# Performance work log

Measured on AMD Instinct MI355X. Metric: run time of the kernel, lower is better.

Reference implementation:

```python
import jax, jax.numpy as jnp
import numpy as np

N, L, C, NHEAD = 4, 2048, 1024, 8
D = C // NHEAD
EPS_ATTN = 1e-6
EPS_LN = 1e-5


def _w(key, shape, scale=0.02):
    return jax.random.normal(key, shape, dtype=jnp.float32) * scale


def setup_inputs() -> dict:
    key = jax.random.key(0)
    ks = jax.random.split(key, 32)
    inp = {
        'depth_feat': jax.random.normal(ks[0], (N, L, C), dtype=jnp.float32),
        'context_feat': jax.random.normal(ks[1], (N, L, C), dtype=jnp.float32),
        'depth_pos': jax.random.normal(ks[2], (N, L, C), dtype=jnp.float32),
        # encoder params (weights stored [in, out]; y = x @ W)
        'e_wq': _w(ks[3], (C, C)), 'e_wk': _w(ks[4], (C, C)), 'e_wv': _w(ks[5], (C, C)),
        'e_wm': _w(ks[6], (C, C)),
        'e_w1': _w(ks[7], (C, 2 * C)), 'e_w2': _w(ks[8], (2 * C, C)),
        'e_g1': jnp.ones((C,), jnp.float32), 'e_b1': jnp.zeros((C,), jnp.float32),
        'e_g2': jnp.ones((C,), jnp.float32), 'e_b2': jnp.zeros((C,), jnp.float32),
        # decoder params
        'd_wq0': _w(ks[9], (C, C)), 'd_wk0': _w(ks[10], (C, C)), 'd_wv0': _w(ks[11], (C, C)),
        'd_wm0': _w(ks[12], (C, C)),
        'd_wq1': _w(ks[13], (C, C)), 'd_wk1': _w(ks[14], (C, C)), 'd_wv1': _w(ks[15], (C, C)),
        'd_wm1': _w(ks[16], (C, C)),
        'd_w1': _w(ks[17], (C, 2 * C)), 'd_w2': _w(ks[18], (2 * C, C)),
        'd_g0': jnp.ones((C,), jnp.float32), 'd_b0': jnp.zeros((C,), jnp.float32),
        'd_g1': jnp.ones((C,), jnp.float32), 'd_b1': jnp.zeros((C,), jnp.float32),
        'd_g2': jnp.ones((C,), jnp.float32), 'd_b2': jnp.zeros((C,), jnp.float32),
    }
    return inp


def layernorm(x, g, b):
    m = jnp.mean(x, axis=-1, keepdims=True)
    v = jnp.mean(jnp.square(x - m), axis=-1, keepdims=True)
    return (x - m) * jax.lax.rsqrt(v + EPS_LN) * g + b


def linear_attention(q, k, v):
    # q,k,v: [N, L, H, D]; elu+1 feature map, O(L) kernelized attention
    Q = jax.nn.elu(q) + 1.0
    K = jax.nn.elu(k) + 1.0
    vlen = v.shape[1]
    v = v / vlen
    KV = jnp.einsum('nshd,nshv->nhdv', K, v)                    # [N,H,D,D]
    Z = 1.0 / (jnp.einsum('nlhd,nhd->nlh', Q, K.sum(axis=1)) + EPS_ATTN)
    out = jnp.einsum('nlhd,nhdv,nlh->nlhv', Q, KV, Z) * vlen    # [N,L,H,D]
    return out


def heads(x):
    n, l, c = x.shape
    return x.reshape(n, l, NHEAD, D)


def encoder_layer(x, wq, wk, wv, wm, w1, w2, g1, b1, g2, b2):
    n, l, c = x.shape
    msg = linear_attention(heads(x @ wq), heads(x @ wk), heads(x @ wv))
    msg = msg.reshape(n, l, c) @ wm
    x = x + layernorm(msg, g1, b1)
    x = x + layernorm(jax.nn.relu(x @ w1) @ w2, g2, b2)
    return x


def decoder_layer(x, src, wq0, wk0, wv0, wm0, wq1, wk1, wv1, wm1, w1, w2, g0, b0, g1, b1, g2, b2):
    n, l, c = x.shape
    msg = linear_attention(heads(x @ wq0), heads(x @ wk0), heads(x @ wv0))
    msg = msg.reshape(n, l, c) @ wm0
    x = x + layernorm(msg, g0, b0)
    msg = linear_attention(heads(x @ wq1), heads(src @ wk1), heads(src @ wv1))
    msg = msg.reshape(n, l, c) @ wm1
    x = x + layernorm(msg, g1, b1)
    x = x + layernorm(jax.nn.relu(x @ w1) @ w2, g2, b2)
    return x


def reference(depth_feat, context_feat, depth_pos,
              e_wq, e_wk, e_wv, e_wm, e_w1, e_w2, e_g1, e_b1, e_g2, e_b2,
              d_wq0, d_wk0, d_wv0, d_wm0, d_wq1, d_wk1, d_wv1, d_wm1,
              d_w1, d_w2, d_g0, d_b0, d_g1, d_b1, d_g2, d_b2):
    ctx = context_feat + depth_pos
    ctx = encoder_layer(ctx, e_wq, e_wk, e_wv, e_wm, e_w1, e_w2, e_g1, e_b1, e_g2, e_b2)
    out = decoder_layer(depth_feat, ctx,
                        d_wq0, d_wk0, d_wv0, d_wm0,
                        d_wq1, d_wk1, d_wv1, d_wm1,
                        d_w1, d_w2, d_g0, d_b0, d_g1, d_b1, d_g2, d_b2)
    return out
```

## Files before the change

### kernel.cpp

```cpp
#include <hip/hip_runtime.h>
#include <cstdint>

#define N_B 4
#define L_S 2048
#define C_F 1024
#define H_N 8
#define D_H 128
#define M_T (N_B * L_S)

typedef __bf16 bf16;
typedef __bf16 bf16x4 __attribute__((ext_vector_type(4)));
typedef __bf16 bf16x8 __attribute__((ext_vector_type(8)));
typedef float f32x4 __attribute__((ext_vector_type(4)));

typedef __attribute__((address_space(1))) void gvoid_t;
typedef __attribute__((address_space(3))) void lvoid_t;

__device__ __forceinline__ void lds_cp16(void* lds, const void* g) {
    __builtin_amdgcn_global_load_lds((gvoid_t*)g, (lvoid_t*)lds, 16, 0, 0);
}

__device__ __forceinline__ float elup1(float x) {
    return x > 0.0f ? x + 1.0f : __expf(x);
}

__device__ __forceinline__ void load4f(const void* base, size_t e0, int isbf, float* o) {
    if (isbf) {
        bf16x4 v = *(const bf16x4*)((const bf16*)base + e0);
        o[0] = (float)v[0]; o[1] = (float)v[1]; o[2] = (float)v[2]; o[3] = (float)v[3];
    } else {
        float4 v = *(const float4*)((const float*)base + e0);
        o[0] = v.x; o[1] = v.y; o[2] = v.z; o[3] = v.w;
    }
}

__device__ __forceinline__ int xcd_swz(int wgid, int nwg) {
    return (wgid & 7) * (nwg >> 3) + (wgid >> 3);
}

__global__ void detect_dtype(const unsigned int* g1, int* flag) {
    if (threadIdx.x == 0 && blockIdx.x == 0)
        *flag = (g1[0] == 0x3F803F80u) ? 1 : 0;
}

__global__ __launch_bounds__(256) void transpose_any(
        const void* __restrict__ src, bf16* __restrict__ dst,
        int R, int Cc, const int* __restrict__ flagp) {
    const int isbf = *flagp;
    __shared__ bf16 tile[32][33];
    const int bx = blockIdx.x * 32;
    const int by = blockIdx.y * 32;
    const int tx = threadIdx.x & 31;
    const int ty = threadIdx.x >> 5;
#pragma unroll
    for (int i = 0; i < 32; i += 8) {
        size_t ix = (size_t)(by + ty + i) * Cc + bx + tx;
        float v = isbf ? (float)((const bf16*)src)[ix] : ((const float*)src)[ix];
        tile[ty + i][tx] = (bf16)v;
    }
    __syncthreads();
#pragma unroll
    for (int i = 0; i < 32; i += 8)
        dst[(size_t)(bx + ty + i) * R + by + tx] = tile[tx][ty + i];
}

struct TAll {
    const void* src[16];
    unsigned int dstoff[16];
    int R[16];
    int C[16];
    int tile0[17];
};

__global__ __launch_bounds__(256) void transpose_all(
        TAll p, bf16* __restrict__ twall, const int* __restrict__ flagp) {
    const int isbf = *flagp;
    int gid = blockIdx.x;
    int w = 0;
    while (gid >= p.tile0[w + 1]) ++w;
    const int local = gid - p.tile0[w];
    const int R = p.R[w], Cc = p.C[w];
    const int tilesx = Cc >> 5;
    const int bx = (local % tilesx) * 32;
    const int by = (local / tilesx) * 32;
    const void* src = p.src[w];
    bf16* dst = twall + p.dstoff[w];
    __shared__ bf16 tile[32][33];
    const int tx = threadIdx.x & 31;
    const int ty = threadIdx.x >> 5;
#pragma unroll
    for (int i = 0; i < 32; i += 8) {
        size_t ix = (size_t)(by + ty + i) * Cc + bx + tx;
        float v = isbf ? (float)((const bf16*)src)[ix] : ((const float*)src)[ix];
        tile[ty + i][tx] = (bf16)v;
    }
    __syncthreads();
#pragma unroll
    for (int i = 0; i < 32; i += 8)
        dst[(size_t)(bx + ty + i) * R + by + tx] = tile[tx][ty + i];
}

template <int ACT>
__global__ __launch_bounds__(256, 2) void gemm_bt(
        const bf16* __restrict__ A, const bf16* __restrict__ Bt,
        bf16* __restrict__ C, int M, int N, int K) {
    __shared__ bf16 sA[2][128 * 64];
    __shared__ bf16 sB[2][128 * 64];
    const int t = threadIdx.x;
    const int lane = t & 63;
    const int w = t >> 6;
    const int wm = (w >> 1) * 64, wn = (w & 1) * 64;
    const int lr = lane & 15, lq = lane >> 4;
    const int gx = gridDim.x;
    const int nwg = gx * gridDim.y;
    const int wgid = xcd_swz(blockIdx.y * gx + blockIdx.x, nwg);
    const int m0 = (wgid / gx) * 128, n0 = (wgid % gx) * 128;

    const bf16* Ab = A + (size_t)m0 * K;
    const bf16* Bb = Bt + (size_t)n0 * K;

    f32x4 acc[4][4] = {};

#define GSTAGE(buf, kt)                                                       \
    {                                                                         \
        _Pragma("unroll")                                                     \
        for (int i_ = 0; i_ < 4; ++i_) {                                      \
            int ci_ = t + i_ * 256;                                           \
            int r_ = ci_ >> 3, c8_ = (ci_ & 7) * 8;                           \
            lds_cp16(&sA[buf][ci_ * 8], Ab + (size_t)r_ * K + (kt) + c8_);    \
        }                                                                     \
        _Pragma("unroll")                                                     \
        for (int i_ = 0; i_ < 4; ++i_) {                                      \
            int ci_ = t + i_ * 256;                                           \
            int r_ = ci_ >> 3, c8_ = (ci_ & 7) * 8;                           \
            lds_cp16(&sB[buf][ci_ * 8], Bb + (size_t)r_ * K + (kt) + c8_);    \
        }                                                                     \
    }

    GSTAGE(0, 0)
    __syncthreads();

    int b = 0;
    for (int kt = 0; kt < K; kt += 64, b ^= 1) {
        if (kt + 64 < K) GSTAGE(b ^ 1, kt + 64)
#pragma unroll
        for (int kk = 0; kk < 64; kk += 32) {
            bf16x8 af[4], bfr[4];
#pragma unroll
            for (int mi = 0; mi < 4; ++mi)
                af[mi] = *(const bf16x8*)&sA[b][(wm + mi * 16 + lr) * 64 + kk + lq * 8];
#pragma unroll
            for (int ni = 0; ni < 4; ++ni)
                bfr[ni] = *(const bf16x8*)&sB[b][(wn + ni * 16 + lr) * 64 + kk + lq * 8];
#pragma unroll
            for (int mi = 0; mi < 4; ++mi)
#pragma unroll
                for (int ni = 0; ni < 4; ++ni)
                    acc[mi][ni] = __builtin_amdgcn_mfma_f32_16x16x32_bf16(
                        af[mi], bfr[ni], acc[mi][ni], 0, 0, 0);
        }
        __syncthreads();
    }
#undef GSTAGE
#pragma unroll
    for (int mi = 0; mi < 4; ++mi)
#pragma unroll
        for (int ni = 0; ni < 4; ++ni)
#pragma unroll
            for (int r = 0; r < 4; ++r) {
                int row = m0 + wm + mi * 16 + lq * 4 + r;
                int col = n0 + wn + ni * 16 + lr;
                float v = acc[mi][ni][r];
                if (ACT == 1) v = fmaxf(v, 0.0f);
                if (ACT == 2) v = v > 0.0f ? v + 1.0f : __expf(v);
                C[(size_t)row * N + col] = (bf16)v;
            }
}

#define STAGE_T(sarr, Gbase, ldstride, Tt)                                    \
    {                                                                         \
        const int sl_ = (Tt) & 3;                                             \
        _Pragma("unroll")                                                     \
        for (int i_ = 0; i_ < 2; ++i_) {                                      \
            int ci_ = t + i_ * 512;                                           \
            int r_ = ci_ >> 2, c8_ = (ci_ & 3) * 8;                           \
            lds_cp16(&sarr[sl_ * 8192 + ci_ * 8],                             \
                     (Gbase) + (size_t)r_ * (ldstride) + ((Tt) << 5) +        \
                         (c8_ ^ ((r_ & 3) << 3)));                            \
        }                                                                     \
    }

template <int ACT>
__global__ __launch_bounds__(512, 2) void gemm256(
        const bf16* __restrict__ A, const bf16* __restrict__ Bt,
        bf16* __restrict__ C, int M, int N, int K, int actsplit) {
    __shared__ bf16 sA[4 * 256 * 32];
    __shared__ bf16 sB[4 * 256 * 32];
    const int t = threadIdx.x;
    const int lane = t & 63;
    const int w = t >> 6;
    const int wr = w >> 2, wc = w & 3;
    const int lr = lane & 15, lq = lane >> 4;
    const int gx = gridDim.x;
    const int nwg = gx * gridDim.y;
    const int wgid = xcd_swz(blockIdx.y * gx + blockIdx.x, nwg);
    const int m0 = (wgid / gx) * 256, n0 = (wgid % gx) * 256;
    const int nt = K >> 5;

    const bf16* Ab = A + (size_t)m0 * K;
    const bf16* Bb = Bt + (size_t)n0 * K;

    f32x4 acc[8][4] = {};

    STAGE_T(sA, Ab, K, 0); STAGE_T(sB, Bb, K, 0);
    STAGE_T(sA, Ab, K, 1); STAGE_T(sB, Bb, K, 1);
    asm volatile("s_waitcnt vmcnt(4)" ::: "memory");
    __builtin_amdgcn_s_barrier();

    for (int T = 0; T < nt; ++T) {
        const bf16* sAs = &sA[(T & 3) * 8192];
        const bf16* sBs = &sB[(T & 3) * 8192];
        bf16x8 af[4], bfr[4], ag[4];
#pragma unroll
        for (int mi = 0; mi < 4; ++mi) {
            int row = wr * 128 + mi * 16 + lr;
            af[mi] = *(const bf16x8*)&sAs[row * 32 + ((lq * 8) ^ ((row & 3) << 3))];
        }
#pragma unroll
        for (int ni = 0; ni < 4; ++ni) {
            int row = wc * 64 + ni * 16 + lr;
            bfr[ni] = *(const bf16x8*)&sBs[row * 32 + ((lq * 8) ^ ((row & 3) << 3))];
        }
        if (T + 2 < nt) STAGE_T(sA, Ab, K, T + 2);
        __builtin_amdgcn_s_barrier();
        __builtin_amdgcn_s_setprio(1);
#pragma unroll
        for (int mi = 0; mi < 4; ++mi)
#pragma unroll
            for (int ni = 0; ni < 4; ++ni)
                acc[mi][ni] = __builtin_amdgcn_mfma_f32_16x16x32_bf16(
                    af[mi], bfr[ni], acc[mi][ni], 0, 0, 0);
        __builtin_amdgcn_s_setprio(0);
        __builtin_amdgcn_s_barrier();
#pragma unroll
        for (int mi = 0; mi < 4; ++mi) {
            int row = wr * 128 + (mi + 4) * 16 + lr;
            ag[mi] = *(const bf16x8*)&sAs[row * 32 + ((lq * 8) ^ ((row & 3) << 3))];
        }
        if (T + 2 < nt) STAGE_T(sB, Bb, K, T + 2);
        __builtin_amdgcn_s_barrier();
        __builtin_amdgcn_s_setprio(1);
#pragma unroll
        for (int mi = 0; mi < 4; ++mi)
#pragma unroll
            for (int ni = 0; ni < 4; ++ni)
                acc[mi + 4][ni] = __builtin_amdgcn_mfma_f32_16x16x32_bf16(
                    ag[mi], bfr[ni], acc[mi + 4][ni], 0, 0, 0);
        __builtin_amdgcn_s_setprio(0);
        if (T + 1 < nt) {
            if (T + 2 < nt) asm volatile("s_waitcnt vmcnt(4)" ::: "memory");
            else            asm volatile("s_waitcnt vmcnt(0)" ::: "memory");
        }
        __builtin_amdgcn_s_barrier();
    }
#pragma unroll
    for (int mi = 0; mi < 8; ++mi)
#pragma unroll
        for (int ni = 0; ni < 4; ++ni)
#pragma unroll
            for (int r = 0; r < 4; ++r) {
                int row = m0 + wr * 128 + mi * 16 + lq * 4 + r;
                int col = n0 + wc * 64 + ni * 16 + lr;
                float v = acc[mi][ni][r];
                if (ACT == 1) v = fmaxf(v, 0.0f);
                if (ACT == 3 && row < actsplit) v = v > 0.0f ? v + 1.0f : __expf(v);
                C[(size_t)row * N + col] = (bf16)v;
            }
}

__global__ __launch_bounds__(256, 2) void attn_kv_mfma(
        const bf16* __restrict__ ktg, const bf16* __restrict__ vtg,
        bf16* __restrict__ KVp, float* __restrict__ KSp) {
    const int nh = blockIdx.x;
    const int chunk = blockIdx.y;
    const int n = nh >> 3, h = nh & 7;
    const int t = threadIdx.x;
    const int lane = t & 63;
    const int w = t >> 6;
    const int wm = (w >> 1) * 64, wn = (w & 1) * 64;
    const int lr = lane & 15, lq = lane >> 4;
    __shared__ bf16 sA[2][128 * 64];
    __shared__ bf16 sB[2][128 * 64];
    const size_t base = (size_t)(h * D_H) * M_T + (size_t)n * L_S + chunk * 128;
    const bf16* Ag0 = vtg + base;
    const bf16* Bg0 = ktg + base;

    f32x4 acc[4][4] = {};
    float ks = 0.0f;
    const int dh = t >> 1, half = (t & 1) * 32;

#define KVSTG(buf, kt)                                                        \
    {                                                                         \
        _Pragma("unroll")                                                     \
        for (int i_ = 0; i_ < 4; ++i_) {                                      \
            int ci_ = t + i_ * 256;                                           \
            int r_ = ci_ >> 3, c8_ = (ci_ & 7) * 8;                           \
            lds_cp16(&sA[buf][ci_ * 8], Ag0 + (size_t)r_ * M_T + (kt) + c8_); \
        }                                                                     \
        _Pragma("unroll")                                                     \
        for (int i_ = 0; i_ < 4; ++i_) {                                      \
            int ci_ = t + i_ * 256;                                           \
            int r_ = ci_ >> 3, c8_ = (ci_ & 7) * 8;                           \
            lds_cp16(&sB[buf][ci_ * 8], Bg0 + (size_t)r_ * M_T + (kt) + c8_); \
        }                                                                     \
    }

    KVSTG(0, 0)
    __syncthreads();

    int b = 0;
    for (int kt = 0; kt < 128; kt += 64, b ^= 1) {
        if (kt + 64 < 128) KVSTG(b ^ 1, kt + 64)
#pragma unroll
        for (int j = 0; j < 4; ++j) {
            bf16x8 v = *(const bf16x8*)&sB[b][dh * 64 + half + j * 8];
#pragma unroll
            for (int m = 0; m < 8; ++m) ks += (float)v[m];
        }
#pragma unroll
        for (int kk = 0; kk < 64; kk += 32) {
            bf16x8 af[4], bfr[4];
#pragma unroll
            for (int mi = 0; mi < 4; ++mi)
                af[mi] = *(const bf16x8*)&sA[b][(wm + mi * 16 + lr) * 64 + kk + lq * 8];
#pragma unroll
            for (int ni = 0; ni < 4; ++ni)
                bfr[ni] = *(const bf16x8*)&sB[b][(wn + ni * 16 + lr) * 64 + kk + lq * 8];
#pragma unroll
            for (int mi = 0; mi < 4; ++mi)
#pragma unroll
                for (int ni = 0; ni < 4; ++ni)
                    acc[mi][ni] = __builtin_amdgcn_mfma_f32_16x16x32_bf16(
                        af[mi], bfr[ni], acc[mi][ni], 0, 0, 0);
        }
        __syncthreads();
    }
#undef KVSTG
    float ko = __shfl_xor(ks, 1);
    if (!(t & 1)) KSp[(nh * 16 + chunk) * D_H + dh] = ks + ko;

    bf16* out = KVp + ((size_t)(nh * 16 + chunk)) * (D_H * D_H);
#pragma unroll
    for (int mi = 0; mi < 4; ++mi)
#pragma unroll
        for (int ni = 0; ni < 4; ++ni)
#pragma unroll
            for (int r = 0; r < 4; ++r) {
                int row = wm + mi * 16 + lq * 4 + r;
                int col = wn + ni * 16 + lr;
                out[(size_t)row * D_H + col] = (bf16)acc[mi][ni][r];
            }
}

__global__ __launch_bounds__(256) void attn_reduce_t(
        const bf16* __restrict__ KVp, const float* __restrict__ KSp,
        bf16* __restrict__ KVt, float* __restrict__ Ksum) {
    const int nh = blockIdx.x;
    const int es = blockIdx.y;
    const int t = threadIdx.x;
    const size_t base = (size_t)nh * 16 * (D_H * D_H) + es * 4096 + t * 16;
    float fa[16] = {};
    for (int c = 0; c < 16; ++c) {
        const bf16* p = KVp + base + (size_t)c * (D_H * D_H);
        bf16x8 a = *(const bf16x8*)p;
        bf16x8 b = *(const bf16x8*)(p + 8);
#pragma unroll
        for (int m = 0; m < 8; ++m) { fa[m] += (float)a[m]; fa[8 + m] += (float)b[m]; }
    }
    bf16* o = KVt + (size_t)nh * (D_H * D_H) + es * 4096 + t * 16;
    bf16x8 oa, ob;
#pragma unroll
    for (int m = 0; m < 8; ++m) { oa[m] = (bf16)fa[m]; ob[m] = (bf16)fa[8 + m]; }
    *(bf16x8*)o = oa;
    *(bf16x8*)(o + 8) = ob;
    if (es == 0 && t < 128) {
        float s = 0.0f;
#pragma unroll
        for (int c = 0; c < 16; ++c) s += KSp[(nh * 16 + c) * D_H + t];
        Ksum[nh * D_H + t] = s;
    }
}

__global__ __launch_bounds__(256, 2) void attn_out_mfma(
        const bf16* __restrict__ qb, const bf16* __restrict__ KVt,
        const float* __restrict__ Ksum, bf16* __restrict__ ab) {
    const int nh = blockIdx.x, tile = blockIdx.y;
    const int n = nh >> 3, h = nh & 7;
    const int t = threadIdx.x;
    const int lane = t & 63;
    const int w = t >> 6;
    const int wm = (w >> 1) * 64, wn = (w & 1) * 64;
    const int lr = lane & 15, lq = lane >> 4;
    __shared__ bf16 sA[2][128 * 64];
    __shared__ bf16 sB[2][128 * 64];
    __shared__ float sKs[128];
    __shared__ float sZp[128][2];
    __shared__ float sZ[128];
    if (t < 128) sKs[t] = Ksum[nh * D_H + t];

    f32x4 acc[4][4] = {};
    float zacc = 0.0f;
    const int zrow = t >> 1, zoff = (t & 1) * 32;
    const size_t qbase = ((size_t)(n * L_S + tile * 128)) * C_F + h * D_H;
    const bf16* Bg0 = KVt + (size_t)nh * (D_H * D_H);

#define OSTG(buf, kt)                                                         \
    {                                                                         \
        _Pragma("unroll")                                                     \
        for (int i_ = 0; i_ < 4; ++i_) {                                      \
            int ci_ = t + i_ * 256;                                           \
            int r_ = ci_ >> 3, c8_ = (ci_ & 7) * 8;                           \
            lds_cp16(&sA[buf][ci_ * 8],                                       \
                     qb + qbase + (size_t)r_ * C_F + (kt) + c8_);             \
            lds_cp16(&sB[buf][ci_ * 8], Bg0 + (size_t)r_ * D_H + (kt) + c8_); \
        }                                                                     \
    }

    OSTG(0, 0)
    __syncthreads();

    int b = 0;
    for (int kt = 0; kt < 128; kt += 64, b ^= 1) {
        if (kt + 64 < 128) OSTG(b ^ 1, kt + 64)
#pragma unroll 8
        for (int j = 0; j < 32; ++j)
            zacc += (float)sA[b][zrow * 64 + zoff + j] * sKs[kt + zoff + j];
#pragma unroll
        for (int kk = 0; kk < 64; kk += 32) {
            bf16x8 af[4], bfr[4];
#pragma unroll
            for (int mi = 0; mi < 4; ++mi)
                af[mi] = *(const bf16x8*)&sA[b][(wm + mi * 16 + lr) * 64 + kk + lq * 8];
#pragma unroll
            for (int ni = 0; ni < 4; ++ni)
                bfr[ni] = *(const bf16x8*)&sB[b][(wn + ni * 16 + lr) * 64 + kk + lq * 8];
#pragma unroll
            for (int mi = 0; mi < 4; ++mi)
#pragma unroll
                for (int ni = 0; ni < 4; ++ni)
                    acc[mi][ni] = __builtin_amdgcn_mfma_f32_16x16x32_bf16(
                        af[mi], bfr[ni], acc[mi][ni], 0, 0, 0);
        }
        __syncthreads();
    }
#undef OSTG
    sZp[zrow][t & 1] = zacc;
    __syncthreads();
    if (t < 128) sZ[t] = 1.0f / (sZp[t][0] + sZp[t][1] + 1e-6f);
    __syncthreads();
#pragma unroll
    for (int mi = 0; mi < 4; ++mi)
#pragma unroll
        for (int ni = 0; ni < 4; ++ni)
#pragma unroll
            for (int r = 0; r < 4; ++r) {
                int row = wm + mi * 16 + lq * 4 + r;
                int col = wn + ni * 16 + lr;
                ab[qbase + (size_t)row * C_F + col] = (bf16)(acc[mi][ni][r] * sZ[row]);
            }
}

template <int F32OUT>
__global__ __launch_bounds__(256) void ln_res(
        const bf16* __restrict__ msg, const void* __restrict__ g,
        const void* __restrict__ bb, const int* __restrict__ flagp,
        const bf16* __restrict__ xin, void* __restrict__ xout) {
    const int isbf = *flagp;
    const int row = blockIdx.x * 4 + (threadIdx.x >> 6);
    const int lane = threadIdx.x & 63;
    const size_t base = (size_t)row * C_F;
    float m[16];
#pragma unroll
    for (int k = 0; k < 4; ++k) {
        bf16x4 v = *(const bf16x4*)(msg + base + k * 256 + lane * 4);
        m[k * 4 + 0] = (float)v[0]; m[k * 4 + 1] = (float)v[1];
        m[k * 4 + 2] = (float)v[2]; m[k * 4 + 3] = (float)v[3];
    }
    float s1 = 0.0f, s2 = 0.0f;
#pragma unroll
    for (int q = 0; q < 16; ++q) { s1 += m[q]; s2 += m[q] * m[q]; }
#pragma unroll
    for (int off = 32; off > 0; off >>= 1) {
        s1 += __shfl_down(s1, off);
        s2 += __shfl_down(s2, off);
    }
    s1 = __shfl(s1, 0);
    s2 = __shfl(s2, 0);
    const float mean = s1 / C_F;
    const float rs = rsqrtf(s2 / C_F - mean * mean + 1e-5f);
#pragma unroll
    for (int k = 0; k < 4; ++k) {
        const size_t cix = k * 256 + lane * 4;
        float ga[4], ba[4];
        load4f(g, cix, isbf, ga);
        load4f(bb, cix, isbf, ba);
        bf16x4 x4 = *(const bf16x4*)(xin + base + cix);
        if (F32OUT) {
            float4 of;
            of.x = (float)x4[0] + (m[k * 4 + 0] - mean) * rs * ga[0] + ba[0];
            of.y = (float)x4[1] + (m[k * 4 + 1] - mean) * rs * ga[1] + ba[1];
            of.z = (float)x4[2] + (m[k * 4 + 2] - mean) * rs * ga[2] + ba[2];
            of.w = (float)x4[3] + (m[k * 4 + 3] - mean) * rs * ga[3] + ba[3];
            *(float4*)((float*)xout + base + cix) = of;
        } else {
            bf16x4 ob;
            ob[0] = (bf16)((float)x4[0] + (m[k * 4 + 0] - mean) * rs * ga[0] + ba[0]);
            ob[1] = (bf16)((float)x4[1] + (m[k * 4 + 1] - mean) * rs * ga[1] + ba[1]);
            ob[2] = (bf16)((float)x4[2] + (m[k * 4 + 2] - mean) * rs * ga[2] + ba[2]);
            ob[3] = (bf16)((float)x4[3] + (m[k * 4 + 3] - mean) * rs * ga[3] + ba[3]);
            *(bf16x4*)((bf16*)xout + base + cix) = ob;
        }
    }
}

__global__ __launch_bounds__(256) void init_ctx_kernel(
        const void* __restrict__ a, const void* __restrict__ b,
        const int* __restrict__ flagp, bf16* __restrict__ xb) {
    const int isbf = *flagp;
    const size_t i = ((size_t)blockIdx.x * 256 + threadIdx.x) * 4;
    float av[4], bv[4];
    load4f(a, i, isbf, av);
    load4f(b, i, isbf, bv);
    bf16x4 o;
#pragma unroll
    for (int q = 0; q < 4; ++q) o[q] = (bf16)(av[q] + bv[q]);
    *(bf16x4*)(xb + i) = o;
}

__global__ __launch_bounds__(256) void conv_copy_kernel(
        const void* __restrict__ a, const int* __restrict__ flagp,
        bf16* __restrict__ xb) {
    const int isbf = *flagp;
    const size_t i = ((size_t)blockIdx.x * 256 + threadIdx.x) * 4;
    float av[4];
    load4f(a, i, isbf, av);
    bf16x4 o;
#pragma unroll
    for (int q = 0; q < 4; ++q) o[q] = (bf16)av[q];
    *(bf16x4*)(xb + i) = o;
}

extern "C" void kernel_launch(void* const* d_in, const int* in_sizes, int n_in,
                              void* d_out, int out_size, void* d_ws, size_t ws_size,
                              hipStream_t stream) {
    const size_t MB = 1u << 20;
    uint8_t* W = (uint8_t*)d_ws;
    bf16* xb    = (bf16*)(W + 0);
    bf16* ctxb  = (bf16*)(W + 16 * MB);
    bf16* qb    = (bf16*)(W + 32 * MB);
    bf16* kb    = (bf16*)(W + 48 * MB);
    bf16* vb    = (bf16*)(W + 64 * MB);
    bf16* hb    = kb;
    bf16* S     = (bf16*)(W + 80 * MB);
    bf16* TW    = (bf16*)(W + 96 * MB);
    bf16* KVp   = S;
    float* KSp  = (float*)(W + 100 * MB);
    bf16* KVt   = (bf16*)(W + 101 * MB);
    float* Ksum = (float*)(W + 102 * MB);
    int*   flag = (int*)(W + 102 * MB + 64 * 1024);
    bf16* TWall = (bf16*)(W + 104 * MB);
    const bool batched = (ws_size >= 145 * MB);

    detect_dtype<<<1, 64, 0, stream>>>((const unsigned int*)d_in[9], flag);

    const int widx[16] = {3,4,5,6,7,8,13,14,15,16,17,18,19,20,21,22};
    const int wR[16]   = {1024,1024,1024,1024,1024,2048,1024,1024,1024,1024,
                          1024,1024,1024,1024,1024,2048};
    const int wC[16]   = {1024,1024,1024,1024,2048,1024,1024,1024,1024,1024,
                          1024,1024,1024,1024,2048,1024};
    unsigned int off[16];
    {
        unsigned int acc = 0;
        for (int i = 0; i < 16; ++i) { off[i] = acc; acc += (unsigned int)wR[i] * wC[i]; }
    }
    if (batched) {
        TAll p;
        int tacc = 0;
        for (int i = 0; i < 16; ++i) {
            p.src[i] = d_in[widx[i]];
            p.dstoff[i] = off[i];
            p.R[i] = wR[i];
            p.C[i] = wC[i];
            p.tile0[i] = tacc;
            tacc += (wR[i] / 32) * (wC[i] / 32);
        }
        p.tile0[16] = tacc;
        transpose_all<<<tacc, 256, 0, stream>>>(p, TWall, flag);
    }
    auto SLOT = [&](int idx) {
        for (int i = 0; i < 16; ++i) if (widx[i] == idx) return i;
        return 0;
    };
    auto BT = [&](int idx) -> const bf16* {
        int s = SLOT(idx);
        if (batched) return TWall + off[s];
        dim3 g(wC[s] / 32, wR[s] / 32);
        transpose_any<<<g, 256, 0, stream>>>(d_in[idx], TW, wR[s], wC[s], flag);
        return TW;
    };
    auto TG = [&](int idx, const bf16* A, bf16* Cc, int Nn, int Kk, int act) {
        const bf16* Bt = BT(idx);
        dim3 g(Nn / 128, M_T / 128);
        if (act == 1)      gemm_bt<1><<<g, 256, 0, stream>>>(A, Bt, Cc, M_T, Nn, Kk);
        else if (act == 2) gemm_bt<2><<<g, 256, 0, stream>>>(A, Bt, Cc, M_T, Nn, Kk);
        else               gemm_bt<0><<<g, 256, 0, stream>>>(A, Bt, Cc, M_T, Nn, Kk);
    };
    auto KVF = [&](int kidx, int vidx, const bf16* X) {
        const bf16* Wt;
        if (batched) {
            Wt = TWall + off[SLOT(kidx)];
        } else {
            dim3 g(32, 32);
            transpose_any<<<g, 256, 0, stream>>>(d_in[kidx], TW, 1024, 1024, flag);
            transpose_any<<<g, 256, 0, stream>>>(d_in[vidx], TW + 1024 * 1024, 1024, 1024, flag);
            Wt = TW;
        }
        dim3 g(M_T / 256, (2 * C_F) / 256);
        gemm256<3><<<g, 512, 0, stream>>>(Wt, X, kb, 2 * C_F, M_T, C_F, C_F);
    };
    auto FFN1 = [&](int idx, const bf16* A) {
        const bf16* Bt = BT(idx);
        dim3 g((2 * C_F) / 256, M_T / 256);
        gemm256<1><<<g, 512, 0, stream>>>(A, Bt, hb, M_T, 2 * C_F, C_F, 0);
    };
    auto ATT = [&](const bf16* q, const bf16* k, const bf16* v, bf16* o) {
        attn_kv_mfma<<<dim3(32, 16), 256, 0, stream>>>(k, v, KVp, KSp);
        attn_reduce_t<<<dim3(32, 4), 256, 0, stream>>>(KVp, KSp, KVt, Ksum);
        attn_out_mfma<<<dim3(32, 16), 256, 0, stream>>>(q, KVt, Ksum, o);
    };
    auto LN = [&](const bf16* m, int gi, int bi, const bf16* xi, bf16* xo) {
        ln_res<0><<<M_T / 4, 256, 0, stream>>>(m, d_in[gi], d_in[bi], flag, xi, (void*)xo);
    };

    init_ctx_kernel<<<M_T * C_F / 1024, 256, 0, stream>>>(d_in[1], d_in[2], flag, xb);
    TG(3, xb, qb, C_F, C_F, 2);
    KVF(4, 5, xb);
    ATT(qb, kb, vb, S);
    TG(6, S, qb, C_F, C_F, 0);
    LN(qb, 9, 10, xb, xb);
    FFN1(7, xb);
    TG(8, hb, S, C_F, 2 * C_F, 0);
    LN(S, 11, 12, xb, ctxb);

    conv_copy_kernel<<<M_T * C_F / 1024, 256, 0, stream>>>(d_in[0], flag, xb);
    TG(13, xb, qb, C_F, C_F, 2);
    KVF(14, 15, xb);
    ATT(qb, kb, vb, S);
    TG(16, S, qb, C_F, C_F, 0);
    LN(qb, 23, 24, xb, xb);
    TG(17, xb, qb, C_F, C_F, 2);
    KVF(18, 19, ctxb);
    ATT(qb, kb, vb, S);
    TG(20, S, qb, C_F, C_F, 0);
    LN(qb, 25, 26, xb, xb);
    FFN1(21, xb);
    TG(22, hb, S, C_F, 2 * C_F, 0);
    ln_res<1><<<M_T / 4, 256, 0, stream>>>(S, d_in[27], d_in[28], flag, xb, d_out);
}
```

Measured before the change: 880.2 us.

## Drop 256-tile GEMM, use 128-tile GEMM with grouped XCD tile mapping everywhere

Removes the 256x256 tile, 512-thread gemm256 kernel and routes the fused K/V projection and FFN1 GEMMs through the 128x128 gemm_bt kernel, which gains the actsplit ELU epilogue. It also replaces the plain XCD swizzle with a grouped tile mapping, so workgroups on the same XCD cover groups of 8 adjacent M tiles for better L2 reuse. The cost is lower per-tile arithmetic intensity and more blocks for those GEMMs, in exchange for better occupancy and cache locality.

```diff
diff --git a/kernel.cpp b/kernel.cpp
--- a/kernel.cpp
+++ b/kernel.cpp
@@ -34,8 +34,16 @@
     }
 }
 
-__device__ __forceinline__ int xcd_swz(int wgid, int nwg) {
-    return (wgid & 7) * (nwg >> 3) + (wgid >> 3);
+__device__ __forceinline__ void tile_map(int orig, int gx, int gy,
+                                         int* mtile, int* ntile) {
+    const int nwg = gx * gy;
+    const int q = nwg >> 3;
+    const int s = (orig & 7) * q + (orig >> 3);
+    const int G = gx << 3;
+    const int g = s / G;
+    const int r = s - g * G;
+    *ntile = r >> 3;
+    *mtile = g * 8 + (r & 7);
 }
 
 __global__ void detect_dtype(const unsigned int* g1, int* flag) {
@@ -103,7 +111,7 @@
 template <int ACT>
 __global__ __launch_bounds__(256, 2) void gemm_bt(
         const bf16* __restrict__ A, const bf16* __restrict__ Bt,
-        bf16* __restrict__ C, int M, int N, int K) {
+        bf16* __restrict__ C, int M, int N, int K, int actsplit) {
     __shared__ bf16 sA[2][128 * 64];
     __shared__ bf16 sB[2][128 * 64];
     const int t = threadIdx.x;
@@ -111,10 +119,9 @@
     const int w = t >> 6;
     const int wm = (w >> 1) * 64, wn = (w & 1) * 64;
     const int lr = lane & 15, lq = lane >> 4;
-    const int gx = gridDim.x;
-    const int nwg = gx * gridDim.y;
-    const int wgid = xcd_swz(blockIdx.y * gx + blockIdx.x, nwg);
-    const int m0 = (wgid / gx) * 128, n0 = (wgid % gx) * 128;
+    int mt, nt_;
+    tile_map(blockIdx.y * gridDim.x + blockIdx.x, gridDim.x, gridDim.y, &mt, &nt_);
+    const int m0 = mt * 128, n0 = nt_ * 128;
 
     const bf16* Ab = A + (size_t)m0 * K;
     const bf16* Bb = Bt + (size_t)n0 * K;
@@ -173,106 +180,6 @@
                 float v = acc[mi][ni][r];
                 if (ACT == 1) v = fmaxf(v, 0.0f);
                 if (ACT == 2) v = v > 0.0f ? v + 1.0f : __expf(v);
-                C[(size_t)row * N + col] = (bf16)v;
-            }
-}
-
-#define STAGE_T(sarr, Gbase, ldstride, Tt)                                    \
-    {                                                                         \
-        const int sl_ = (Tt) & 3;                                             \
-        _Pragma("unroll")                                                     \
-        for (int i_ = 0; i_ < 2; ++i_) {                                      \
-            int ci_ = t + i_ * 512;                                           \
-            int r_ = ci_ >> 2, c8_ = (ci_ & 3) * 8;                           \
-            lds_cp16(&sarr[sl_ * 8192 + ci_ * 8],                             \
-                     (Gbase) + (size_t)r_ * (ldstride) + ((Tt) << 5) +        \
-                         (c8_ ^ ((r_ & 3) << 3)));                            \
-        }                                                                     \
-    }
-
-template <int ACT>
-__global__ __launch_bounds__(512, 2) void gemm256(
-        const bf16* __restrict__ A, const bf16* __restrict__ Bt,
-        bf16* __restrict__ C, int M, int N, int K, int actsplit) {
-    __shared__ bf16 sA[4 * 256 * 32];
-    __shared__ bf16 sB[4 * 256 * 32];
-    const int t = threadIdx.x;
-    const int lane = t & 63;
-    const int w = t >> 6;
-    const int wr = w >> 2, wc = w & 3;
-    const int lr = lane & 15, lq = lane >> 4;
-    const int gx = gridDim.x;
-    const int nwg = gx * gridDim.y;
-    const int wgid = xcd_swz(blockIdx.y * gx + blockIdx.x, nwg);
-    const int m0 = (wgid / gx) * 256, n0 = (wgid % gx) * 256;
-    const int nt = K >> 5;
-
-    const bf16* Ab = A + (size_t)m0 * K;
-    const bf16* Bb = Bt + (size_t)n0 * K;
-
-    f32x4 acc[8][4] = {};
-
-    STAGE_T(sA, Ab, K, 0); STAGE_T(sB, Bb, K, 0);
-    STAGE_T(sA, Ab, K, 1); STAGE_T(sB, Bb, K, 1);
-    asm volatile("s_waitcnt vmcnt(4)" ::: "memory");
-    __builtin_amdgcn_s_barrier();
-
-    for (int T = 0; T < nt; ++T) {
-        const bf16* sAs = &sA[(T & 3) * 8192];
-        const bf16* sBs = &sB[(T & 3) * 8192];
-        bf16x8 af[4], bfr[4], ag[4];
-#pragma unroll
-        for (int mi = 0; mi < 4; ++mi) {
-            int row = wr * 128 + mi * 16 + lr;
-            af[mi] = *(const bf16x8*)&sAs[row * 32 + ((lq * 8) ^ ((row & 3) << 3))];
-        }
-#pragma unroll
-        for (int ni = 0; ni < 4; ++ni) {
-            int row = wc * 64 + ni * 16 + lr;
-            bfr[ni] = *(const bf16x8*)&sBs[row * 32 + ((lq * 8) ^ ((row & 3) << 3))];
-        }
-        if (T + 2 < nt) STAGE_T(sA, Ab, K, T + 2);
-        __builtin_amdgcn_s_barrier();
-        __builtin_amdgcn_s_setprio(1);
-#pragma unroll
-        for (int mi = 0; mi < 4; ++mi)
-#pragma unroll
-            for (int ni = 0; ni < 4; ++ni)
-                acc[mi][ni] = __builtin_amdgcn_mfma_f32_16x16x32_bf16(
-                    af[mi], bfr[ni], acc[mi][ni], 0, 0, 0);
-        __builtin_amdgcn_s_setprio(0);
-        __builtin_amdgcn_s_barrier();
-#pragma unroll
-        for (int mi = 0; mi < 4; ++mi) {
-            int row = wr * 128 + (mi + 4) * 16 + lr;
-            ag[mi] = *(const bf16x8*)&sAs[row * 32 + ((lq * 8) ^ ((row & 3) << 3))];
-        }
-        if (T + 2 < nt) STAGE_T(sB, Bb, K, T + 2);
-        __builtin_amdgcn_s_barrier();
-        __builtin_amdgcn_s_setprio(1);
-#pragma unroll
-        for (int mi = 0; mi < 4; ++mi)
-#pragma unroll
-            for (int ni = 0; ni < 4; ++ni)
-                acc[mi + 4][ni] = __builtin_amdgcn_mfma_f32_16x16x32_bf16(
-                    ag[mi], bfr[ni], acc[mi + 4][ni], 0, 0, 0);
-        __builtin_amdgcn_s_setprio(0);
-        if (T + 1 < nt) {
-            if (T + 2 < nt) asm volatile("s_waitcnt vmcnt(4)" ::: "memory");
-            else            asm volatile("s_waitcnt vmcnt(0)" ::: "memory");
-        }
-        __builtin_amdgcn_s_barrier();
-    }
-#pragma unroll
-    for (int mi = 0; mi < 8; ++mi)
-#pragma unroll
-        for (int ni = 0; ni < 4; ++ni)
-#pragma unroll
-            for (int r = 0; r < 4; ++r) {
-                int row = m0 + wr * 128 + mi * 16 + lq * 4 + r;
-                int col = n0 + wc * 64 + ni * 16 + lr;
-                float v = acc[mi][ni][r];
-                if (ACT == 1) v = fmaxf(v, 0.0f);
                 if (ACT == 3 && row < actsplit) v = v > 0.0f ? v + 1.0f : __expf(v);
                 C[(size_t)row * N + col] = (bf16)v;
             }
@@ -611,9 +518,9 @@
     auto TG = [&](int idx, const bf16* A, bf16* Cc, int Nn, int Kk, int act) {
         const bf16* Bt = BT(idx);
         dim3 g(Nn / 128, M_T / 128);
-        if (act == 1)      gemm_bt<1><<<g, 256, 0, stream>>>(A, Bt, Cc, M_T, Nn, Kk);
-        else if (act == 2) gemm_bt<2><<<g, 256, 0, stream>>>(A, Bt, Cc, M_T, Nn, Kk);
-        else               gemm_bt<0><<<g, 256, 0, stream>>>(A, Bt, Cc, M_T, Nn, Kk);
+        if (act == 1)      gemm_bt<1><<<g, 256, 0, stream>>>(A, Bt, Cc, M_T, Nn, Kk, 0);
+        else if (act == 2) gemm_bt<2><<<g, 256, 0, stream>>>(A, Bt, Cc, M_T, Nn, Kk, 0);
+        else               gemm_bt<0><<<g, 256, 0, stream>>>(A, Bt, Cc, M_T, Nn, Kk, 0);
     };
     auto KVF = [&](int kidx, int vidx, const bf16* X) {
         const bf16* Wt;
@@ -625,13 +532,8 @@
             transpose_any<<<g, 256, 0, stream>>>(d_in[vidx], TW + 1024 * 1024, 1024, 1024, flag);
             Wt = TW;
         }
-        dim3 g(M_T / 256, (2 * C_F) / 256);
-        gemm256<3><<<g, 512, 0, stream>>>(Wt, X, kb, 2 * C_F, M_T, C_F, C_F);
-    };
-    auto FFN1 = [&](int idx, const bf16* A) {
-        const bf16* Bt = BT(idx);
-        dim3 g((2 * C_F) / 256, M_T / 256);
-        gemm256<1><<<g, 512, 0, stream>>>(A, Bt, hb, M_T, 2 * C_F, C_F, 0);
+        dim3 g(M_T / 128, (2 * C_F) / 128);
+        gemm_bt<3><<<g, 256, 0, stream>>>(Wt, X, kb, 2 * C_F, M_T, C_F, C_F);
     };
     auto ATT = [&](const bf16* q, const bf16* k, const bf16* v, bf16* o) {
         attn_kv_mfma<<<dim3(32, 16), 256, 0, stream>>>(k, v, KVp, KSp);
@@ -648,7 +550,7 @@
     ATT(qb, kb, vb, S);
     TG(6, S, qb, C_F, C_F, 0);
     LN(qb, 9, 10, xb, xb);
-    FFN1(7, xb);
+    TG(7, xb, hb, 2 * C_F, C_F, 1);
     TG(8, hb, S, C_F, 2 * C_F, 0);
     LN(S, 11, 12, xb, ctxb);
 
@@ -663,7 +565,7 @@
     ATT(qb, kb, vb, S);
     TG(20, S, qb, C_F, C_F, 0);
     LN(qb, 25, 26, xb, xb);
-    FFN1(21, xb);
+    TG(21, xb, hb, 2 * C_F, C_F, 1);
     TG(22, hb, S, C_F, 2 * C_F, 0);
     ln_res<1><<<M_T / 4, 256, 0, stream>>>(S, d_in[27], d_in[28], flag, xb, d_out);
 }
```

New measurement: 952.1 us. 1.08x slower.
